# Performance work log

Measured on AMD Instinct MI355X. Metric: run time of the kernel, lower is better.

## Reference

```python
import jax, jax.numpy as jnp
import numpy as np

EPS = 2e-5
N_ROT = 4  # p4 group: rotations by multiples of 90 degrees (exact via rot90)


def _conv2d(x, w, pad):
    # x: [B, Cin, H, W], w: [Cout, Cin, k, k]
    return jax.lax.conv_general_dilated(
        x, w, window_strides=(1, 1), padding=[(pad, pad), (pad, pad)],
        dimension_numbers=('NCHW', 'OIHW', 'NCHW'))


def _conv_rng(x, w):
    # Lifting (Rn -> G) conv. x: [B, I, H, W], w: [O, I, k, k] -> [B, O, 4, H', W']
    O, I, k, _ = w.shape
    wr = jnp.stack([jnp.rot90(w, r, axes=(-2, -1)) for r in range(N_ROT)])  # [4,O,I,k,k]
    y = _conv2d(x, wr.reshape(N_ROT * O, I, k, k), 0)  # [B, 4*O, H', W']
    B, _, H2, W2 = y.shape
    return y.reshape(B, N_ROT, O, H2, W2).transpose(0, 2, 1, 3, 4)


def _conv_gg(x, w, pad=0):
    # Group (G -> G) conv. x: [B, I, 4, H, W], w: [O, I, 4, k, k] -> [B, O, 4, H', W']
    O, I, _, k, _ = w.shape
    ws = []
    for r in range(N_ROT):
        wr = jnp.rot90(w, r, axes=(-2, -1))      # spatial rotation of the kernel
        wr = jnp.roll(wr, r, axis=2)              # cyclic shift of orientation axis
        ws.append(wr.reshape(O, I * N_ROT, k, k))
    wall = jnp.concatenate(ws, 0)                 # [4*O, I*4, k, k]
    B = x.shape[0]
    y = _conv2d(x.reshape(B, I * N_ROT, x.shape[-2], x.shape[-1]), wall, pad)
    H2, W2 = y.shape[-2:]
    return y.reshape(B, N_ROT, O, H2, W2).transpose(0, 2, 1, 3, 4)


def _att_rng(x, aw):
    # fSpatialAttention on Rn input: channel avg+max pooling -> 7x7 conv -> sigmoid gate.
    # x: [B, C, H, W], aw: [1, 2, 7, 7]
    pooled = jnp.concatenate([x.mean(1, keepdims=True), x.max(1, keepdims=True)], axis=1)
    att = jax.nn.sigmoid(_conv2d(pooled, aw, 3))  # [B,1,H,W], SAME padding
    return x * att


def _att_gg(x, aw):
    # fSpatialAttentionGG on G input: channel avg+max pooling -> equivariant 7x7 GG conv -> sigmoid.
    # x: [B, C, 4, H, W], aw: [1, 2, 4, 7, 7]
    pooled = jnp.concatenate([x.mean(1, keepdims=True), x.max(1, keepdims=True)], axis=1)
    att = jax.nn.sigmoid(_conv_gg(pooled, aw, pad=3))  # [B,1,4,H,W]
    return x * att


def _bn(x, g, b):
    # BatchNorm3d over [B, C, 4, H, W]: per-channel stats over (B, 4, H, W)
    m = x.mean((0, 2, 3, 4), keepdims=True)
    v = x.var((0, 2, 3, 4), keepdims=True)
    return (x - m) * jax.lax.rsqrt(v + EPS) * g.reshape(1, -1, 1, 1, 1) + b.reshape(1, -1, 1, 1, 1)


def _pool(x):
    # max_pooling_Rn: 2x2/2 spatial max pool applied independently per orientation
    return jax.lax.reduce_window(x, -jnp.inf, jax.lax.max,
                                 (1, 1, 1, 2, 2), (1, 1, 1, 2, 2), 'VALID')


def setup_inputs() -> dict:
    key = jax.random.key(0)
    ks = jax.random.split(key, 40)
    B, C = 2048, 10
    d = {'x': jax.random.normal(ks[0], (B, 1, 28, 28), jnp.float32)}
    d['c1_w'] = 0.2 * jax.random.normal(ks[1], (C, 1, 3, 3), jnp.float32)
    d['a1_w'] = 0.1 * jax.random.normal(ks[2], (1, 2, 7, 7), jnp.float32)
    j = 3
    for i in range(2, 7):
        d['c%d_w' % i] = 0.1 * jax.random.normal(ks[j], (C, C, 4, 3, 3), jnp.float32); j += 1
        d['a%d_w' % i] = 0.1 * jax.random.normal(ks[j], (1, 2, 4, 7, 7), jnp.float32); j += 1
    d['c7_w'] = 0.1 * jax.random.normal(ks[j], (10, C, 4, 4, 4), jnp.float32); j += 1
    d['a7_w'] = 0.1 * jax.random.normal(ks[j], (1, 2, 4, 7, 7), jnp.float32); j += 1
    for i in range(1, 7):
        d['bn%d_g' % i] = jnp.ones((C,), jnp.float32)
        d['bn%d_b' % i] = jnp.zeros((C,), jnp.float32)
    return d


def reference(x, c1_w, a1_w, c2_w, a2_w, c3_w, a3_w, c4_w, a4_w, c5_w, a5_w,
              c6_w, a6_w, c7_w, a7_w, bn1_g, bn1_b, bn2_g, bn2_b, bn3_g, bn3_b,
              bn4_g, bn4_b, bn5_g, bn5_b, bn6_g, bn6_b):
    # Dropout is treated as identity (eval mode / deterministic reference).
    out = jax.nn.relu(_bn(_conv_rng(_att_rng(x, a1_w), c1_w), bn1_g, bn1_b))      # [B,10,4,26,26]
    out = jax.nn.relu(_bn(_conv_gg(_att_gg(out, a2_w), c2_w), bn2_g, bn2_b))       # [B,10,4,24,24]
    out = _pool(out)                                                                # [B,10,4,12,12]
    out = jax.nn.relu(_bn(_conv_gg(_att_gg(out, a3_w), c3_w), bn3_g, bn3_b))       # 10x10
    out = jax.nn.relu(_bn(_conv_gg(_att_gg(out, a4_w), c4_w), bn4_g, bn4_b))       # 8x8
    out = jax.nn.relu(_bn(_conv_gg(_att_gg(out, a5_w), c5_w), bn5_g, bn5_b))       # 6x6
    out = jax.nn.relu(_bn(_conv_gg(_att_gg(out, a6_w), c6_w), bn6_g, bn6_b))       # 4x4
    out = _conv_gg(_att_gg(out, a7_w), c7_w)                                        # [B,10,4,1,1]
    out = out.max(axis=2)                                                           # group max-pool over orientations
    return out.reshape(out.shape[0], 10)
```

## Files before the change

kernel.cpp:

```cpp
#include <hip/hip_runtime.h>
#include <hip/hip_bf16.h>
#include <cstddef>

typedef __hip_bfloat16 bf;
typedef __attribute__((ext_vector_type(8))) short short8x;
typedef __attribute__((ext_vector_type(4))) float f32x4;

__device__ __forceinline__ float ldv(const float* p){ return *p; }
__device__ __forceinline__ float ldv(const bf* p){ return __bfloat162float(*p); }
__device__ __forceinline__ void stv(float* p, float v){ *p = v; }
__device__ __forceinline__ void stv(bf* p, float v){ *p = __float2bfloat16(v); }
__device__ __forceinline__ float sigm(float x){ return 1.f/(1.f + __expf(-x)); }
__device__ __forceinline__ short bfbits(float v){
  __hip_bfloat16 h = __float2bfloat16(v);
  return *(short*)&h;
}

__device__ __forceinline__ float ldin(const void* p, long i, int f32){
  return f32 ? ((const float*)p)[i] : __bfloat162float(((const bf*)p)[i]);
}

template<int K>
__device__ __forceinline__ int rot_src(int r, int t){
  int u = t / K, v = t % K;
  int s1 = v*K + (K-1-u);
  int s2 = (K-1-u)*K + (K-1-v);
  int s3 = (K-1-v)*K + u;
  return r==0 ? t : (r==1 ? s1 : (r==2 ? s2 : s3));
}

__device__ __forceinline__ void finalize10(const float* ssum, const float* ssq,
                                           const void* g, const void* bb, int f32, float invN,
                                           float* scs, float* shs, int tid){
  if (tid < 10){
    float m = ssum[tid] * invN;
    float v = fmaxf(ssq[tid] * invN - m*m, 0.f);
    float sc = ldin(g, tid, f32) * rsqrtf(v + 2e-5f);
    scs[tid] = sc;
    shs[tid] = ldin(bb, tid, f32) - m * sc;
  }
}

__global__ void k_detect(const void* x, int* ctrl){
  int lane = threadIdx.x;
  float mx = 0.f;
  for (int i = lane; i < 2048; i += 64){
    float v = __bfloat162float(((const bf*)x)[i]);
    if (v != v) v = 1e30f;
    mx = fmaxf(mx, fabsf(v));
  }
  #pragma unroll
  for (int off = 32; off > 0; off >>= 1) mx = fmaxf(mx, __shfl_xor(mx, off));
  if (lane == 0) ctrl[0] = (mx > 1e6f) ? 1 : 0;
}

__global__ __launch_bounds__(256) void k_build_bt(const void* c2, const void* c3, const void* c4,
                                                  const int* __restrict__ ctrl, short* __restrict__ btg){
  const void* ws[3] = {c2, c3, c4};
  const void* cw = ws[blockIdx.x];
  short* outp = btg + blockIdx.x * 18432;
  int f32 = ctrl[0];
  for (int i = threadIdx.x; i < 18432; i += 256){
    int t, n, k;
    bool valid;
    if (i < 13824){
      t = i / 1536;
      int rem = i % 1536;
      int kq = rem / 384;
      n = (i >> 3) % 48;
      k = kq*8 + (i & 7);
      valid = (n < 40);
    } else {
      int j2 = i - 13824;
      int tg = j2 / 1536;
      int lq = (j2 % 1536) / 384;
      n = (j2 >> 3) % 48;
      k = 32 + (i & 7);
      t = tg*4 + lq;
      valid = (t < 9) && (n < 40);
    }
    float v = 0.f;
    if (valid){
      int o = n >> 2, r = n & 3, ci = k >> 2, s = k & 3;
      v = ldin(cw, ((o*10 + ci)*4 + ((s - r) & 3))*9 + rot_src<3>(r, t), f32);
    }
    outp[i] = bfbits(v);
  }
}

__global__ __launch_bounds__(256) void k_l1(const void* __restrict__ x,
                                            const void* __restrict__ a1,
                                            const void* __restrict__ c1,
                                            const int* __restrict__ ctrl,
                                            float* __restrict__ xa,
                                            float* __restrict__ ssum, float* __restrict__ ssq){
  __shared__ float xs[784];
  __shared__ float ws[49];
  __shared__ float xg[28*29];
  __shared__ float wr1[360];
  __shared__ float lsum[16], lss[16];
  int b = blockIdx.x, tid = threadIdx.x;
  int f32 = ctrl[0];
  for (int i = tid; i < 784; i += 256) xs[i] = ldin(x, (long)b*784 + i, f32);
  if (tid < 49) ws[tid] = ldin(a1, tid, f32) + ldin(a1, 49 + tid, f32);
  for (int i = tid; i < 360; i += 256){
    int r = i / 90, rem = i % 90, o = rem / 9, t = rem % 9;
    wr1[i] = ldin(c1, o*9 + rot_src<3>(r, t), f32);
  }
  if (tid < 16){ lsum[tid] = 0.f; lss[tid] = 0.f; }
  __syncthreads();
  for (int p = tid; p < 784; p += 256){
    int h = p / 28, w = p % 28;
    float acc = 0.f;
    #pragma unroll
    for (int u = 0; u < 7; ++u){
      int hh = h + u - 3;
      if (hh < 0 || hh >= 28) continue;
      #pragma unroll
      for (int v = 0; v < 7; ++v){
        int ww = w + v - 3;
        if (ww < 0 || ww >= 28) continue;
        acc = fmaf(xs[hh*28 + ww], ws[u*7 + v], acc);
      }
    }
    float g = xs[p] * sigm(acc);
    xg[h*29 + w] = g;
    xa[(size_t)b*784 + p] = g;
  }
  __syncthreads();
  for (int it = tid; it < 1040; it += 256){
    int o = it / 104, rem = it % 104, r = rem / 26, h = rem % 26;
    float wt[9];
    #pragma unroll
    for (int t = 0; t < 9; ++t) wt[t] = wr1[(r*10 + o)*9 + t];
    float acc[26];
    #pragma unroll
    for (int w = 0; w < 26; ++w) acc[w] = 0.f;
    #pragma unroll
    for (int u = 0; u < 3; ++u){
      float rr[28];
      #pragma unroll
      for (int j = 0; j < 28; ++j) rr[j] = xg[(h + u)*29 + j];
      #pragma unroll
      for (int v = 0; v < 3; ++v){
        float wv = wt[u*3 + v];
        #pragma unroll
        for (int w = 0; w < 26; ++w) acc[w] = fmaf(rr[w + v], wv, acc[w]);
      }
    }
    float s1 = 0.f, s2 = 0.f;
    #pragma unroll
    for (int w = 0; w < 26; ++w){ s1 += acc[w]; s2 += acc[w]*acc[w]; }
    atomicAdd(&lsum[o], s1); atomicAdd(&lss[o], s2);
  }
  __syncthreads();
  if (tid < 10){ atomicAdd(&ssum[tid], lsum[tid]); atomicAdd(&ssq[tid], lss[tid]); }
}

__global__ __launch_bounds__(128) void k_att2(const float* __restrict__ xa,
                                              const void* __restrict__ c1,
                                              const float* __restrict__ pss, const float* __restrict__ psq,
                                              const void* __restrict__ pg, const void* __restrict__ pb,
                                              float pinvN,
                                              const void* __restrict__ aw,
                                              const int* __restrict__ ctrl,
                                              float* __restrict__ attf){
  __shared__ float xs[28*29];
  __shared__ float wr1[360];
  __shared__ float ps[8*26*33];
  __shared__ float wl[1568];
  __shared__ float scs[10], shs[10];
  int b = blockIdx.x, tid = threadIdx.x;
  int f32 = ctrl[0];
  for (int i = tid; i < 784; i += 128){
    int row = i / 28, col = i % 28;
    xs[row*29 + col] = xa[(size_t)b*784 + i];
  }
  for (int i = tid; i < 360; i += 128){
    int r = i / 90, rem = i % 90, o = rem / 9, t = rem % 9;
    wr1[i] = ldin(c1, o*9 + rot_src<3>(r, t), f32);
  }
  for (int i = tid; i < 8*26*33; i += 128) ps[i] = 0.f;
  for (int i = tid; i < 1568; i += 128){
    int r = i / 392, rem = i % 392, i2 = rem / 196, s = (rem % 196)/49, t = rem % 49;
    int sp = (s - r) & 3;
    wl[i] = ldin(aw, (i2*4 + sp)*49 + rot_src<7>(r, t), f32);
  }
  finalize10(pss, psq, pg, pb, f32, pinvN, scs, shs, tid);
  __syncthreads();
  if (tid < 104){
    int s = tid / 26, h = tid % 26;
    float msum[26], mmax[26];
    #pragma unroll
    for (int w = 0; w < 26; ++w){ msum[w] = 0.f; mmax[w] = 0.f; }
    for (int o = 0; o < 10; ++o){
      const float* wb = wr1 + (s*10 + o)*9;
      float acc[26];
      #pragma unroll
      for (int w = 0; w < 26; ++w) acc[w] = 0.f;
      #pragma unroll
      for (int u = 0; u < 3; ++u){
        float rr[28];
        #pragma unroll
        for (int j = 0; j < 28; ++j) rr[j] = xs[(h + u)*29 + j];
        #pragma unroll
        for (int v = 0; v < 3; ++v){
          float wv = wb[u*3 + v];
          #pragma unroll
          for (int w = 0; w < 26; ++w) acc[w] = fmaf(rr[w + v], wv, acc[w]);
        }
      }
      float a_sc = scs[o], a_sh = shs[o];
      #pragma unroll
      for (int w = 0; w < 26; ++w){
        float val = fmaxf(fmaf(acc[w], a_sc, a_sh), 0.f);
        msum[w] += val; mmax[w] = fmaxf(mmax[w], val);
      }
    }
    #pragma unroll
    for (int w = 0; w < 26; ++w){
      ps[s*858 + h*33 + 3 + w] = msum[w] * 0.1f;
      ps[(4 + s)*858 + h*33 + 3 + w] = mmax[w];
    }
  }
  __syncthreads();
  if (tid < 104){
    int r = tid / 26, h = tid % 26;
    float acc[26];
    #pragma unroll
    for (int w = 0; w < 26; ++w) acc[w] = 0.f;
    for (int c = 0; c < 8; ++c){
      const float* wb = wl + r*392 + c*49;
      const float* pb2 = ps + c*858;
      #pragma unroll
      for (int u = 0; u < 7; ++u){
        int row = h + u - 3;
        if (row < 0 || row >= 26) continue;
        float rr[32];
        #pragma unroll
        for (int j = 0; j < 32; ++j) rr[j] = pb2[row*33 + j];
        #pragma unroll
        for (int v = 0; v < 7; ++v){
          float wv = wb[u*7 + v];
          #pragma unroll
          for (int w = 0; w < 26; ++w) acc[w] = fmaf(rr[w + v], wv, acc[w]);
        }
      }
    }
    size_t base = ((size_t)b*4 + r)*676 + (size_t)h*26;
    #pragma unroll
    for (int w = 0; w < 26; ++w) attf[base + w] = sigm(acc[w]);
  }
}

__global__ __launch_bounds__(512, 4) void k_conv2m(const float* __restrict__ xa,
                                                const void* __restrict__ c1,
                                                const float* __restrict__ pss, const float* __restrict__ psq,
                                                const void* __restrict__ pg, const void* __restrict__ pb,
                                                float pinvN,
                                                const float* __restrict__ attm,
                                                const short* __restrict__ btg,
                                                const int* __restrict__ ctrl,
                                                bf* __restrict__ ap2,
                                                float* __restrict__ ssum, float* __restrict__ ssq){
  __shared__ alignas(16) float xs2[784];
  __shared__ float wr1[360];
  __shared__ alignas(16) float attL[4*676];
  __shared__ alignas(16) short xin[676*40];
  __shared__ float scs[10], shs[10];
  __shared__ float lsum[16], lss[16];
  int tid = threadIdx.x, b = blockIdx.x;
  int f32 = ctrl[0];
  for (int i = tid; i < 784; i += 512) xs2[i] = xa[(size_t)b*784 + i];
  for (int i = tid; i < 360; i += 512){
    int r = i / 90, rem = i % 90, o = rem / 9, t = rem % 9;
    wr1[i] = ldin(c1, o*9 + rot_src<3>(r, t), f32);
  }
  for (int i = tid; i < 2704; i += 512) attL[i] = attm[(size_t)b*2704 + i];
  finalize10(pss, psq, pg, pb, f32, pinvN, scs, shs, tid);
  if (tid < 16){ lsum[tid] = 0.f; lss[tid] = 0.f; }
  __syncthreads();
  for (int it = tid; it < 1040; it += 512){
    int row = it / 40, ch = it % 40;
    int ci = ch >> 2, s = ch & 3;
    float wt[9];
    {
      const float* wb = wr1 + (s*10 + ci)*9;
      #pragma unroll
      for (int t = 0; t < 9; ++t) wt[t] = wb[t];
    }
    float sc = scs[ci], sh = shs[ci];
    float acc[26];
    #pragma unroll
    for (int w = 0; w < 26; ++w) acc[w] = 0.f;
    #pragma unroll
    for (int u = 0; u < 3; ++u){
      float rr[28];
      const float4* rp = (const float4*)(xs2 + (row + u)*28);
      #pragma unroll
      for (int j = 0; j < 7; ++j){ float4 q = rp[j]; rr[4*j]=q.x; rr[4*j+1]=q.y; rr[4*j+2]=q.z; rr[4*j+3]=q.w; }
      #pragma unroll
      for (int v = 0; v < 3; ++v){
        float wv = wt[u*3 + v];
        #pragma unroll
        for (int w = 0; w < 26; ++w) acc[w] = fmaf(rr[w + v], wv, acc[w]);
      }
    }
    const float* ap = attL + s*676 + row*26;
    int chv = ch >> 3, chl = ch & 7;
    #pragma unroll
    for (int w = 0; w < 26; ++w){
      float v = fmaxf(fmaf(acc[w], sc, sh), 0.f) * ap[w];
      int sp = row*26 + w;
      int phys = (ch < 32) ? sp*40 + (((chv + (sp>>3)) & 3) << 3) + chl
                           : sp*40 + ch;
      xin[phys] = bfbits(v);
    }
  }
  __syncthreads();

  int wv = tid >> 6, lane = tid & 63, lm = lane & 15, lq = lane >> 4;
  short8x bmain[9], btail[3];
  int tdh[3], tdw[3];
  #pragma unroll
  for (int tg = 0; tg < 3; ++tg){
    int tap = tg*4 + lq; if (tap > 8) tap = 8;
    tdh[tg] = tap / 3; tdw[tg] = tap % 3;
  }
  int curNt = -1, n = 0, o = 0;
  for (int u = wv; u < 54; u += 8){
    int nt = u / 18, mp = u % 18;
    if (nt != curNt){
      curNt = nt; n = nt*16 + lm; o = n >> 2;
      #pragma unroll
      for (int t = 0; t < 9; ++t)
        bmain[t] = *(const short8x*)(btg + (((t*4 + lq)*48 + n) << 3));
      #pragma unroll
      for (int tg = 0; tg < 3; ++tg)
        btail[tg] = *(const short8x*)(btg + 13824 + (((tg*4 + lq)*48 + n) << 3));
    }
    int mt0 = mp*2, mt1 = mp*2 + 1;
    int mA0 = mt0*16 + lm, mA1 = mt1*16 + lm;
    int qi0 = mA0 >> 2, sub0 = mA0 & 3;
    int h00 = 2*(qi0/12) + (sub0 >> 1), w00 = 2*(qi0%12) + (sub0 & 1);
    int qi1 = mA1 >> 2, sub1 = mA1 & 3;
    int h01 = 2*(qi1/12) + (sub1 >> 1), w01 = 2*(qi1%12) + (sub1 & 1);
    f32x4 acc0 = {0.f,0.f,0.f,0.f}, acc1 = {0.f,0.f,0.f,0.f};
    #pragma unroll
    for (int t = 0; t < 9; ++t){
      int sp0 = (h00 + t/3)*26 + (w00 + t%3);
      int sp1 = (h01 + t/3)*26 + (w01 + t%3);
      short8x a0 = *(const short8x*)&xin[sp0*40 + (((lq + (sp0>>3)) & 3) << 3)];
      short8x a1 = *(const short8x*)&xin[sp1*40 + (((lq + (sp1>>3)) & 3) << 3)];
      acc0 = __builtin_amdgcn_mfma_f32_16x16x32_bf16(a0, bmain[t], acc0, 0, 0, 0);
      acc1 = __builtin_amdgcn_mfma_f32_16x16x32_bf16(a1, bmain[t], acc1, 0, 0, 0);
    }
    #pragma unroll
    for (int tg = 0; tg < 3; ++tg){
      int sp0 = (h00 + tdh[tg])*26 + (w00 + tdw[tg]);
      int sp1 = (h01 + tdh[tg])*26 + (w01 + tdw[tg]);
      short8x a0 = *(const short8x*)&xin[sp0*40 + 32];
      short8x a1 = *(const short8x*)&xin[sp1*40 + 32];
      acc0 = __builtin_amdgcn_mfma_f32_16x16x32_bf16(a0, btail[tg], acc0, 0, 0, 0);
      acc1 = __builtin_amdgcn_mfma_f32_16x16x32_bf16(a1, btail[tg], acc1, 0, 0, 0);
    }
    if (n < 40){
      float s1 = acc0[0]+acc0[1]+acc0[2]+acc0[3] + acc1[0]+acc1[1]+acc1[2]+acc1[3];
      float s2 = acc0[0]*acc0[0]+acc0[1]*acc0[1]+acc0[2]*acc0[2]+acc0[3]*acc0[3]
               + acc1[0]*acc1[0]+acc1[1]*acc1[1]+acc1[2]*acc1[2]+acc1[3]*acc1[3];
      atomicAdd(&lsum[o], s1); atomicAdd(&lss[o], s2);
      float mx0 = fmaxf(fmaxf(acc0[0], acc0[1]), fmaxf(acc0[2], acc0[3]));
      float mx1 = fmaxf(fmaxf(acc1[0], acc1[1]), fmaxf(acc1[2], acc1[3]));
      size_t pbase = ((size_t)b*40 + n)*144;
      stv(ap2 + pbase + mt0*4 + lq, mx0);
      stv(ap2 + pbase + mt1*4 + lq, mx1);
    }
  }
  __syncthreads();
  if (tid < 10){ atomicAdd(&ssum[tid], lsum[tid]); atomicAdd(&ssq[tid], lss[tid]); }
}

template<int HIN, int WIN, int NT, typename TI>
__global__ __launch_bounds__(NT) void k_conv_ggm(const TI* __restrict__ act,
                                                 const float* __restrict__ pss, const float* __restrict__ psq,
                                                 const void* __restrict__ pg, const void* __restrict__ pb,
                                                 float pinvN,
                                                 const float* __restrict__ attm,
                                                 const short* __restrict__ btg,
                                                 const int* __restrict__ ctrl,
                                                 float* __restrict__ out,
                                                 float* __restrict__ ssum, float* __restrict__ ssq){
  constexpr int HOUT = HIN - 2, WOUT = WIN - 2;
  constexpr int M = HOUT*WOUT, HW = HIN*WIN;
  constexpr int MT = (M + 15)/16, MU = (MT + 1)/2, UNITS = MU*3;
  constexpr int NWV = NT/64;
  __shared__ alignas(16) short xin[HW*40];
  __shared__ float scs[10], shs[10];
  __shared__ float lsum[16], lss[16];
  int tid = threadIdx.x, b = blockIdx.x;
  int f32 = ctrl[0];
  if (tid < 16){ lsum[tid] = 0.f; lss[tid] = 0.f; }
  finalize10(pss, psq, pg, pb, f32, pinvN, scs, shs, tid);
  __syncthreads();
  for (int i = tid; i < HW*40; i += NT){
    int sp = i / 40, ch = i % 40;
    int ci = ch >> 2, s = ch & 3;
    float a = ldv(act + ((size_t)b*40 + ch)*HW + sp);
    a = fmaxf(fmaf(a, scs[ci], shs[ci]), 0.f);
    float v = a * attm[((size_t)b*4 + s)*HW + sp];
    int phys = (ch < 32) ? sp*40 + ((((ch>>3) + (sp>>3)) & 3) << 3) + (ch & 7)
                         : sp*40 + ch;
    xin[phys] = bfbits(v);
  }
  __syncthreads();
  int wv = tid >> 6, lane = tid & 63, lm = lane & 15, lq = lane >> 4;
  short8x bmain[9], btail[3];
  int tdh[3], tdw[3];
  #pragma unroll
  for (int tg = 0; tg < 3; ++tg){
    int tap = tg*4 + lq; if (tap > 8) tap = 8;
    tdh[tg] = tap / 3; tdw[tg] = tap % 3;
  }
  int curNt = -1, n = 0, o = 0;
  for (int u = wv; u < UNITS; u += NWV){
    int nt = u / MU, mu = u % MU;
    if (nt != curNt){
      curNt = nt; n = nt*16 + lm; o = n >> 2;
      #pragma unroll
      for (int t = 0; t < 9; ++t)
        bmain[t] = *(const short8x*)(btg + (((t*4 + lq)*48 + n) << 3));
      #pragma unroll
      for (int tg = 0; tg < 3; ++tg)
        btail[tg] = *(const short8x*)(btg + 13824 + (((tg*4 + lq)*48 + n) << 3));
    }
    int mt0 = mu*2, mt1 = mu*2 + 1;
    int mA0 = mt0*16 + lm; if (mA0 > M-1) mA0 = M-1;
    int mA1 = mt1*16 + lm; if (mA1 > M-1) mA1 = M-1;
    int mh0 = mA0 / WOUT, mw0 = mA0 % WOUT;
    int mh1 = mA1 / WOUT, mw1 = mA1 % WOUT;
    f32x4 acc0 = {0.f,0.f,0.f,0.f}, acc1 = {0.f,0.f,0.f,0.f};
    #pragma unroll
    for (int t = 0; t < 9; ++t){
      int sp0 = (mh0 + t/3)*WIN + (mw0 + t%3);
      int sp1 = (mh1 + t/3)*WIN + (mw1 + t%3);
      short8x a0 = *(const short8x*)&xin[sp0*40 + (((lq + (sp0>>3)) & 3) << 3)];
      short8x a1 = *(const short8x*)&xin[sp1*40 + (((lq + (sp1>>3)) & 3) << 3)];
      acc0 = __builtin_amdgcn_mfma_f32_16x16x32_bf16(a0, bmain[t], acc0, 0, 0, 0);
      acc1 = __builtin_amdgcn_mfma_f32_16x16x32_bf16(a1, bmain[t], acc1, 0, 0, 0);
    }
    #pragma unroll
    for (int tg = 0; tg < 3; ++tg){
      int sp0 = (mh0 + tdh[tg])*WIN + (mw0 + tdw[tg]);
      int sp1 = (mh1 + tdh[tg])*WIN + (mw1 + tdw[tg]);
      short8x a0 = *(const short8x*)&xin[sp0*40 + 32];
      short8x a1 = *(const short8x*)&xin[sp1*40 + 32];
      acc0 = __builtin_amdgcn_mfma_f32_16x16x32_bf16(a0, btail[tg], acc0, 0, 0, 0);
      acc1 = __builtin_amdgcn_mfma_f32_16x16x32_bf16(a1, btail[tg], acc1, 0, 0, 0);
    }
    if (n < 40){
      float s1 = 0.f, s2 = 0.f;
      size_t obase = ((size_t)b*40 + n)*M;
      #pragma unroll
      for (int reg = 0; reg < 4; ++reg){
        int m0 = mt0*16 + lq*4 + reg;
        if (m0 < M){ float v = acc0[reg]; s1 += v; s2 += v*v; out[obase + m0] = v; }
        int m1 = mt1*16 + lq*4 + reg;
        if (m1 < M){ float v = acc1[reg]; s1 += v; s2 += v*v; out[obase + m1] = v; }
      }
      atomicAdd(&lsum[o], s1); atomicAdd(&lss[o], s2);
    }
  }
  __syncthreads();
  if (tid < 10){ atomicAdd(&ssum[tid], lsum[tid]); atomicAdd(&ssq[tid], lss[tid]); }
}

template<int H, int W, int NT, typename TA>
__global__ __launch_bounds__(NT) void k_att_gg(const TA* __restrict__ act,
                                               const float* __restrict__ pss, const float* __restrict__ psq,
                                               const void* __restrict__ pg, const void* __restrict__ pb,
                                               float pinvN,
                                               const void* __restrict__ aw,
                                               const int* __restrict__ ctrl,
                                               float* __restrict__ att){
  constexpr int WG = (W + 6) | 1;
  constexpr int HW = H*W;
  __shared__ float ps[8*H*WG];
  __shared__ float wl[1568];
  __shared__ float scs[10], shs[10];
  int b = blockIdx.x, tid = threadIdx.x;
  int f32 = ctrl[0];
  finalize10(pss, psq, pg, pb, f32, pinvN, scs, shs, tid);
  for (int i = tid; i < 1568; i += NT){
    int r = i / 392, rem = i % 392, i2 = rem / 196, s = (rem % 196)/49, t = rem % 49;
    int sp = (s - r) & 3;
    wl[i] = ldin(aw, (i2*4 + sp)*49 + rot_src<7>(r, t), f32);
  }
  __syncthreads();
  for (int i = tid; i < 4*H*WG; i += NT){
    int s = i / (H*WG), rem = i % (H*WG), row = rem / WG, col = rem % WG;
    int cc = col - 3;
    float mn = 0.f, mx = 0.f;
    if (cc >= 0 && cc < W){
      float sum = 0.f; mx = 0.f;
      const TA* ap = act + (size_t)b*40*HW + (size_t)s*HW + row*W + cc;
      #pragma unroll
      for (int c = 0; c < 10; ++c){
        float v = fmaxf(fmaf(ldv(ap + (size_t)c*4*HW), scs[c], shs[c]), 0.f);
        sum += v; mx = fmaxf(mx, v);
      }
      mn = sum * 0.1f;
    }
    ps[s*H*WG + row*WG + col] = mn;
    ps[(4 + s)*H*WG + row*WG + col] = mx;
  }
  __syncthreads();
  for (int it = tid; it < 4*H; it += NT){
    int r = it / H, h = it % H;
    float acc[W];
    #pragma unroll
    for (int w = 0; w < W; ++w) acc[w] = 0.f;
    for (int c = 0; c < 8; ++c){
      const float* wb = wl + r*392 + c*49;
      const float* pb2 = ps + c*H*WG;
      #pragma unroll
      for (int u = 0; u < 7; ++u){
        int row = h + u - 3;
        if (row < 0 || row >= H) continue;
        float rr[W + 6];
        #pragma unroll
        for (int j = 0; j < W + 6; ++j) rr[j] = pb2[row*WG + j];
        #pragma unroll
        for (int v = 0; v < 7; ++v){
          float wv = wb[u*7 + v];
          #pragma unroll
          for (int w = 0; w < W; ++w) acc[w] = fmaf(rr[w + v], wv, acc[w]);
        }
      }
    }
    size_t base = ((size_t)b*4 + r)*HW + (size_t)h*W;
    #pragma unroll
    for (int w = 0; w < W; ++w) att[base + w] = sigm(acc[w]);
  }
}

template<int HIN, int WIN, int K, int SR, int NT, bool STATS, typename TI, typename TO>
__global__ __launch_bounds__(NT) void k_conv_gg(const TI* __restrict__ act,
                                                const float* __restrict__ pss, const float* __restrict__ psq,
                                                const void* __restrict__ pg, const void* __restrict__ pb,
                                                float pinvN,
                                                const float* __restrict__ attm,
                                                const void* __restrict__ cw,
                                                const int* __restrict__ ctrl,
                                                TO* __restrict__ out,
                                                float* __restrict__ ssum, float* __restrict__ ssq){
  constexpr int HOUT = HIN - K + 1;
  constexpr int WOUT = WIN - K + 1;
  constexpr int NS   = HOUT / SR;
  constexpr int WP   = WIN | 1;
  constexpr int NW   = 10*10*4*K*K;
  __shared__ float xin[40*HIN*WP];
  __shared__ float wl[NW];
  __shared__ float scs[10], shs[10];
  __shared__ float lsum[16], lss[16];
  int tid = threadIdx.x;
  int b = blockIdx.x;
  int f32 = ctrl[0];
  for (int i = tid; i < NW; i += NT) wl[i] = ldin(cw, i, f32);
  finalize10(pss, psq, pg, pb, f32, pinvN, scs, shs, tid);
  if (STATS && tid < 16){ lsum[tid] = 0.f; lss[tid] = 0.f; }
  __syncthreads();
  for (int i = tid; i < 40*HIN*WP; i += NT){
    int c = i / (HIN*WP), rem = i % (HIN*WP), rr = rem / WP, col = rem % WP;
    float v = 0.f;
    if (col < WIN){
      int ch = c >> 2, s = c & 3;
      float a = ldv(act + ((size_t)b*40 + c)*HIN*WIN + (size_t)rr*WIN + col);
      a = fmaxf(fmaf(a, scs[ch], shs[ch]), 0.f);
      v = a * attm[((size_t)b*4 + s)*HIN*WIN + (size_t)rr*WIN + col];
    }
    xin[i] = v;
  }
  __syncthreads();
  for (int it = tid; it < 40*NS; it += NT){
    int o = it / (4*NS), rem = it % (4*NS), r = rem / NS, hs = rem % NS;
    int h0 = hs * SR;
    int perm[K*K];
    #pragma unroll
    for (int t = 0; t < K*K; ++t) perm[t] = rot_src<K>(r, t);
    float acc[SR][WOUT];
    #pragma unroll
    for (int a = 0; a < SR; ++a)
      #pragma unroll
      for (int w = 0; w < WOUT; ++w) acc[a][w] = 0.f;
    for (int ci = 0; ci < 10; ++ci){
      #pragma unroll
      for (int s = 0; s < 4; ++s){
        int sp = (s - r) & 3;
        const float* wb = wl + (size_t)((o*10 + ci)*4 + sp)*K*K;
        float wt[K*K];
        #pragma unroll
        for (int t = 0; t < K*K; ++t) wt[t] = wb[perm[t]];
        const float* ib = xin + (ci*4 + s)*HIN*WP;
        #pragma unroll
        for (int ri = 0; ri < SR + K - 1; ++ri){
          float rr[WP];
          #pragma unroll
          for (int j = 0; j < WP; ++j) rr[j] = ib[(h0 + ri)*WP + j];
          #pragma unroll
          for (int u = 0; u < K; ++u){
            int orr = ri - u;
            if (orr < 0 || orr >= SR) continue;
            #pragma unroll
            for (int v = 0; v < K; ++v){
              float wv = wt[u*K + v];
              #pragma unroll
              for (int w = 0; w < WOUT; ++w) acc[orr][w] = fmaf(rr[w + v], wv, acc[orr][w]);
            }
          }
        }
      }
    }
    if (STATS){
      float s1 = 0.f, s2 = 0.f;
      #pragma unroll
      for (int a = 0; a < SR; ++a)
        #pragma unroll
        for (int w = 0; w < WOUT; ++w){ s1 += acc[a][w]; s2 += acc[a][w]*acc[a][w]; }
      atomicAdd(&lsum[o], s1); atomicAdd(&lss[o], s2);
    }
    #pragma unroll
    for (int a = 0; a < SR; ++a){
      size_t base = ((size_t)b*40 + o*4 + r)*HOUT*WOUT + (size_t)(h0 + a)*WOUT;
      #pragma unroll
      for (int w = 0; w < WOUT; ++w) stv(out + base + w, acc[a][w]);
    }
  }
  if (STATS){
    __syncthreads();
    if (tid < 10){ atomicAdd(&ssum[tid], lsum[tid]); atomicAdd(&ssq[tid], lss[tid]); }
  }
}

__global__ __launch_bounds__(64) void k_conv7(const float* __restrict__ act,
                                              const float* __restrict__ pss, const float* __restrict__ psq,
                                              const void* __restrict__ pg, const void* __restrict__ pb,
                                              float pinvN,
                                              const float* __restrict__ attm,
                                              const void* __restrict__ cw,
                                              const int* __restrict__ ctrl,
                                              void* __restrict__ outp){
  constexpr int WP = 5;
  __shared__ float xin[40*4*WP];
  __shared__ float wl[6400];
  __shared__ float scs[10], shs[10];
  __shared__ float ybuf[48];
  int tid = threadIdx.x, b = blockIdx.x;
  int f32 = ctrl[0];
  for (int i = tid; i < 6400; i += 64) wl[i] = ldin(cw, i, f32);
  finalize10(pss, psq, pg, pb, f32, pinvN, scs, shs, tid);
  __syncthreads();
  for (int i = tid; i < 40*4*WP; i += 64){
    int c = i / (4*WP), rem = i % (4*WP), rr = rem / WP, col = rem % WP;
    float v = 0.f;
    if (col < 4){
      int ch = c >> 2, s = c & 3;
      float a = ldv(act + ((size_t)b*40 + c)*16 + (size_t)rr*4 + col);
      a = fmaxf(fmaf(a, scs[ch], shs[ch]), 0.f);
      v = a * attm[((size_t)b*4 + s)*16 + (size_t)rr*4 + col];
    }
    xin[i] = v;
  }
  __syncthreads();
  if (tid < 40){
    int o = tid >> 2, r = tid & 3;
    int perm[16];
    #pragma unroll
    for (int t = 0; t < 16; ++t) perm[t] = rot_src<4>(r, t);
    float acc = 0.f;
    for (int ci = 0; ci < 10; ++ci){
      #pragma unroll
      for (int s = 0; s < 4; ++s){
        int sp = (s - r) & 3;
        const float* wb = wl + ((o*10 + ci)*4 + sp)*16;
        const float* ib = xin + (ci*4 + s)*4*WP;
        #pragma unroll
        for (int u = 0; u < 4; ++u)
          #pragma unroll
          for (int v = 0; v < 4; ++v)
            acc = fmaf(ib[u*WP + v], wb[perm[u*4 + v]], acc);
      }
    }
    ybuf[tid] = acc;
  }
  __syncthreads();
  if (tid < 10){
    const float* p = ybuf + tid*4;
    float m = fmaxf(fmaxf(p[0], p[1]), fmaxf(p[2], p[3]));
    if (f32) ((float*)outp)[(size_t)b*10 + tid] = m;
    else stv((bf*)outp + (size_t)b*10 + tid, m);
  }
}

extern "C" void kernel_launch(void* const* d_in, const int* in_sizes, int n_in,
                              void* d_out, int out_size, void* d_ws, size_t ws_size,
                              hipStream_t stream){
  (void)in_sizes; (void)n_in; (void)out_size; (void)ws_size;
  const void* x  = d_in[0];
  const void* c1 = d_in[1];
  const void* a1 = d_in[2];
  const void* c2 = d_in[3];
  const void* a2 = d_in[4];
  const void* c3 = d_in[5];
  const void* a3 = d_in[6];
  const void* c4 = d_in[7];
  const void* a4 = d_in[8];
  const void* c5 = d_in[9];
  const void* a5 = d_in[10];
  const void* c6 = d_in[11];
  const void* a6 = d_in[12];
  const void* c7 = d_in[13];
  const void* a7 = d_in[14];
  const void* bng[6] = {d_in[15],d_in[17],d_in[19],d_in[21],d_in[23],d_in[25]};
  const void* bnb[6] = {d_in[16],d_in[18],d_in[20],d_in[22],d_in[24],d_in[26]};

  size_t off = 0;
  char* wsb = (char*)d_ws;
  auto alloc = [&](size_t bytes)->void*{ void* p = wsb + off; off += (bytes + 255) & ~(size_t)255; return p; };
  int*   ctrl   = (int*)alloc(256);
  float* stats  = (float*)alloc(192*sizeof(float));
  short* btfr   = (short*)alloc(3*18432*2);
  char*  region1 = (char*)alloc(28573696);
  bf*    ap2 = (bf*)alloc((size_t)2048*40*144*2);
  float* yD  = (float*)alloc((size_t)2048*40*100*4);
  float* xa    = (float*)region1;
  float* attf2 = (float*)(region1 + 6422528);
  float* yE    = (float*)region1;
  float* attf3 = (float*)(region1 + 20971520);

  const float iN1 = 1.f/5537792.f, iN2 = 1.f/4718592.f, iN3 = 1.f/819200.f;
  const float iN4 = 1.f/524288.f, iN5 = 1.f/294912.f, iN6 = 1.f/131072.f;

  hipMemsetAsync(ctrl, 0, 1024, stream);
  k_detect<<<1, 64, 0, stream>>>(x, ctrl);
  k_build_bt<<<3, 256, 0, stream>>>(c2, c3, c4, ctrl, btfr);

  k_l1<<<2048, 256, 0, stream>>>(x, a1, c1, ctrl, xa, stats + 0, stats + 16);

  k_att2<<<2048, 128, 0, stream>>>(xa, c1, stats + 0, stats + 16, bng[0], bnb[0], iN1, a2, ctrl, attf2);
  k_conv2m<<<2048, 512, 0, stream>>>(xa, c1, stats + 0, stats + 16, bng[0], bnb[0], iN1,
                                     attf2, btfr, ctrl, ap2, stats + 32, stats + 48);

  k_att_gg<12,12,64,bf><<<2048, 64, 0, stream>>>(ap2, stats + 32, stats + 48, bng[1], bnb[1], iN2, a3, ctrl, attf3);
  k_conv_ggm<12,12,256,bf><<<2048, 256, 0, stream>>>(ap2, stats + 32, stats + 48, bng[1], bnb[1], iN2,
                                                     attf3, btfr + 18432, ctrl, yD, stats + 64, stats + 80);

  k_att_gg<10,10,64,float><<<2048, 64, 0, stream>>>(yD, stats + 64, stats + 80, bng[2], bnb[2], iN3, a4, ctrl, attf3);
  k_conv_ggm<10,10,128,float><<<2048, 128, 0, stream>>>(yD, stats + 64, stats + 80, bng[2], bnb[2], iN3,
                                                        attf3, btfr + 36864, ctrl, yE, stats + 96, stats + 112);

  k_att_gg<8,8,64,float><<<2048, 64, 0, stream>>>(yE, stats + 96, stats + 112, bng[3], bnb[3], iN4, a5, ctrl, attf3);
  k_conv_gg<8,8,3,2,192,true,float,float><<<2048, 192, 0, stream>>>(yE, stats + 96, stats + 112, bng[3], bnb[3], iN4,
                                                                attf3, c5, ctrl, yD, stats + 128, stats + 144);

  k_att_gg<6,6,64,float><<<2048, 64, 0, stream>>>(yD, stats + 128, stats + 144, bng[4], bnb[4], iN5, a6, ctrl, attf3);
  k_conv_gg<6,6,3,2,128,true,float,float><<<2048, 128, 0, stream>>>(yD, stats + 128, stats + 144, bng[4], bnb[4], iN5,
                                                                attf3, c6, ctrl, yE, stats + 160, stats + 176);

  k_att_gg<4,4,64,float><<<2048, 64, 0, stream>>>(yE, stats + 160, stats + 176, bng[5], bnb[5], iN6, a7, ctrl, attf3);
  k_conv7<<<2048, 64, 0, stream>>>(yE, stats + 160, stats + 176, bng[5], bnb[5], iN6,
                                   attf3, c7, ctrl, d_out);
}
```

Baseline: 967.5 us.

## Split conv2 kernel into two row halves per image and drop LDS swizzle

k_conv2m now launches two blocks per image, each covering 12 pooled output rows from a 14-row input slab. This shrinks per-block LDS (xin, attL, xs2) so more blocks can be resident, and the launch-bounds occupancy hint is raised to match. The XOR-style channel swizzle in the xin LDS layout is removed in both conv kernels in favour of plain sp*40+ch indexing, which simplifies address math but may bring back LDS bank conflicts on the short8 reads. Halving the work adds duplicated weight and BN-finalize setup per block and doubles the number of global stat atomics.

```diff
diff --git a/kernel.cpp b/kernel.cpp
--- a/kernel.cpp
+++ b/kernel.cpp
@@ -253,7 +253,7 @@
   }
 }
 
-__global__ __launch_bounds__(512, 4) void k_conv2m(const float* __restrict__ xa,
+__global__ __launch_bounds__(512, 8) void k_conv2m(const float* __restrict__ xa,
                                                 const void* __restrict__ c1,
                                                 const float* __restrict__ pss, const float* __restrict__ psq,
                                                 const void* __restrict__ pg, const void* __restrict__ pb,
@@ -263,25 +263,29 @@
                                                 const int* __restrict__ ctrl,
                                                 bf* __restrict__ ap2,
                                                 float* __restrict__ ssum, float* __restrict__ ssq){
-  __shared__ alignas(16) float xs2[784];
+  __shared__ alignas(16) float xs2[16*28];
   __shared__ float wr1[360];
-  __shared__ alignas(16) float attL[4*676];
-  __shared__ alignas(16) short xin[676*40];
+  __shared__ alignas(16) float attL[4*364];
+  __shared__ alignas(16) short xin[364*40];
   __shared__ float scs[10], shs[10];
   __shared__ float lsum[16], lss[16];
-  int tid = threadIdx.x, b = blockIdx.x;
+  int tid = threadIdx.x, b = blockIdx.x >> 1, half = blockIdx.x & 1;
+  int rb = 12*half;
   int f32 = ctrl[0];
-  for (int i = tid; i < 784; i += 512) xs2[i] = xa[(size_t)b*784 + i];
+  for (int i = tid; i < 448; i += 512) xs2[i] = xa[(size_t)b*784 + (size_t)rb*28 + i];
   for (int i = tid; i < 360; i += 512){
     int r = i / 90, rem = i % 90, o = rem / 9, t = rem % 9;
     wr1[i] = ldin(c1, o*9 + rot_src<3>(r, t), f32);
   }
-  for (int i = tid; i < 2704; i += 512) attL[i] = attm[(size_t)b*2704 + i];
+  for (int i = tid; i < 1456; i += 512){
+    int s = i / 364, j = i % 364;
+    attL[i] = attm[(size_t)b*2704 + (size_t)s*676 + rb*26 + j];
+  }
   finalize10(pss, psq, pg, pb, f32, pinvN, scs, shs, tid);
   if (tid < 16){ lsum[tid] = 0.f; lss[tid] = 0.f; }
   __syncthreads();
-  for (int it = tid; it < 1040; it += 512){
-    int row = it / 40, ch = it % 40;
+  for (int it = tid; it < 560; it += 512){
+    int lr = it / 40, ch = it % 40;
     int ci = ch >> 2, s = ch & 3;
     float wt[9];
     {
@@ -296,7 +300,7 @@
     #pragma unroll
     for (int u = 0; u < 3; ++u){
       float rr[28];
-      const float4* rp = (const float4*)(xs2 + (row + u)*28);
+      const float4* rp = (const float4*)(xs2 + (lr + u)*28);
       #pragma unroll
       for (int j = 0; j < 7; ++j){ float4 q = rp[j]; rr[4*j]=q.x; rr[4*j+1]=q.y; rr[4*j+2]=q.z; rr[4*j+3]=q.w; }
       #pragma unroll
@@ -306,15 +310,11 @@
         for (int w = 0; w < 26; ++w) acc[w] = fmaf(rr[w + v], wv, acc[w]);
       }
     }
-    const float* ap = attL + s*676 + row*26;
-    int chv = ch >> 3, chl = ch & 7;
+    const float* ap = attL + s*364 + lr*26;
     #pragma unroll
     for (int w = 0; w < 26; ++w){
       float v = fmaxf(fmaf(acc[w], sc, sh), 0.f) * ap[w];
-      int sp = row*26 + w;
-      int phys = (ch < 32) ? sp*40 + (((chv + (sp>>3)) & 3) << 3) + chl
-                           : sp*40 + ch;
-      xin[phys] = bfbits(v);
+      xin[(lr*26 + w)*40 + ch] = bfbits(v);
     }
   }
   __syncthreads();
@@ -328,8 +328,8 @@
     tdh[tg] = tap / 3; tdw[tg] = tap % 3;
   }
   int curNt = -1, n = 0, o = 0;
-  for (int u = wv; u < 54; u += 8){
-    int nt = u / 18, mp = u % 18;
+  for (int u = wv; u < 27; u += 8){
+    int nt = u / 9, mp = u % 9;
     if (nt != curNt){
       curNt = nt; n = nt*16 + lm; o = n >> 2;
       #pragma unroll
@@ -341,17 +341,17 @@
     }
     int mt0 = mp*2, mt1 = mp*2 + 1;
     int mA0 = mt0*16 + lm, mA1 = mt1*16 + lm;
-    int qi0 = mA0 >> 2, sub0 = mA0 & 3;
-    int h00 = 2*(qi0/12) + (sub0 >> 1), w00 = 2*(qi0%12) + (sub0 & 1);
-    int qi1 = mA1 >> 2, sub1 = mA1 & 3;
-    int h01 = 2*(qi1/12) + (sub1 >> 1), w01 = 2*(qi1%12) + (sub1 & 1);
+    int qg0 = 72*half + (mA0 >> 2), sub0 = mA0 & 3;
+    int h00 = 2*(qg0/12) - rb + (sub0 >> 1), w00 = 2*(qg0%12) + (sub0 & 1);
+    int qg1 = 72*half + (mA1 >> 2), sub1 = mA1 & 3;
+    int h01 = 2*(qg1/12) - rb + (sub1 >> 1), w01 = 2*(qg1%12) + (sub1 & 1);
     f32x4 acc0 = {0.f,0.f,0.f,0.f}, acc1 = {0.f,0.f,0.f,0.f};
     #pragma unroll
     for (int t = 0; t < 9; ++t){
       int sp0 = (h00 + t/3)*26 + (w00 + t%3);
       int sp1 = (h01 + t/3)*26 + (w01 + t%3);
-      short8x a0 = *(const short8x*)&xin[sp0*40 + (((lq + (sp0>>3)) & 3) << 3)];
-      short8x a1 = *(const short8x*)&xin[sp1*40 + (((lq + (sp1>>3)) & 3) << 3)];
+      short8x a0 = *(const short8x*)&xin[sp0*40 + lq*8];
+      short8x a1 = *(const short8x*)&xin[sp1*40 + lq*8];
       acc0 = __builtin_amdgcn_mfma_f32_16x16x32_bf16(a0, bmain[t], acc0, 0, 0, 0);
       acc1 = __builtin_amdgcn_mfma_f32_16x16x32_bf16(a1, bmain[t], acc1, 0, 0, 0);
     }
@@ -372,8 +372,8 @@
       float mx0 = fmaxf(fmaxf(acc0[0], acc0[1]), fmaxf(acc0[2], acc0[3]));
       float mx1 = fmaxf(fmaxf(acc1[0], acc1[1]), fmaxf(acc1[2], acc1[3]));
       size_t pbase = ((size_t)b*40 + n)*144;
-      stv(ap2 + pbase + mt0*4 + lq, mx0);
-      stv(ap2 + pbase + mt1*4 + lq, mx1);
+      stv(ap2 + pbase + 72*half + mt0*4 + lq, mx0);
+      stv(ap2 + pbase + 72*half + mt1*4 + lq, mx1);
     }
   }
   __syncthreads();
@@ -407,10 +407,7 @@
     int ci = ch >> 2, s = ch & 3;
     float a = ldv(act + ((size_t)b*40 + ch)*HW + sp);
     a = fmaxf(fmaf(a, scs[ci], shs[ci]), 0.f);
-    float v = a * attm[((size_t)b*4 + s)*HW + sp];
-    int phys = (ch < 32) ? sp*40 + ((((ch>>3) + (sp>>3)) & 3) << 3) + (ch & 7)
-                         : sp*40 + ch;
-    xin[phys] = bfbits(v);
+    xin[i] = bfbits(a * attm[((size_t)b*4 + s)*HW + sp]);
   }
   __syncthreads();
   int wv = tid >> 6, lane = tid & 63, lm = lane & 15, lq = lane >> 4;
@@ -443,8 +440,8 @@
     for (int t = 0; t < 9; ++t){
       int sp0 = (mh0 + t/3)*WIN + (mw0 + t%3);
       int sp1 = (mh1 + t/3)*WIN + (mw1 + t%3);
-      short8x a0 = *(const short8x*)&xin[sp0*40 + (((lq + (sp0>>3)) & 3) << 3)];
-      short8x a1 = *(const short8x*)&xin[sp1*40 + (((lq + (sp1>>3)) & 3) << 3)];
+      short8x a0 = *(const short8x*)&xin[sp0*40 + lq*8];
+      short8x a1 = *(const short8x*)&xin[sp1*40 + lq*8];
       acc0 = __builtin_amdgcn_mfma_f32_16x16x32_bf16(a0, bmain[t], acc0, 0, 0, 0);
       acc1 = __builtin_amdgcn_mfma_f32_16x16x32_bf16(a1, bmain[t], acc1, 0, 0, 0);
     }
@@ -747,7 +744,7 @@
   k_l1<<<2048, 256, 0, stream>>>(x, a1, c1, ctrl, xa, stats + 0, stats + 16);
 
   k_att2<<<2048, 128, 0, stream>>>(xa, c1, stats + 0, stats + 16, bng[0], bnb[0], iN1, a2, ctrl, attf2);
-  k_conv2m<<<2048, 512, 0, stream>>>(xa, c1, stats + 0, stats + 16, bng[0], bnb[0], iN1,
+  k_conv2m<<<4096, 512, 0, stream>>>(xa, c1, stats + 0, stats + 16, bng[0], bnb[0], iN1,
                                      attf2, btfr, ctrl, ap2, stats + 32, stats + 48);
 
   k_att_gg<12,12,64,bf><<<2048, 64, 0, stream>>>(ap2, stats + 32, stats + 48, bng[1], bnb[1], iN2, a3, ctrl, attf3);
```

After: 1.060 ms. 9.5% more time.
